# Kernel optimization log

Measured on AMD Instinct MI355X. Metric: run time of the kernel, lower is better.

## Reference

```python
import jax, jax.numpy as jnp
import numpy as np

N_MESH, N_GRID, N_EDGES, D, H = 40962, 200000, 600000, 128, 128


def layer_norm(x, g, b, eps=1e-5):
    mu = x.mean(-1, keepdims=True)
    xc = x - mu
    var = (xc * xc).mean(-1, keepdims=True)
    return xc * jax.lax.rsqrt(var + eps) * g + b


def setup_inputs() -> dict:
    key = jax.random.key(0)
    ks = jax.random.split(key, 16)
    s = 1.0 / np.sqrt(D).astype(np.float32)
    s2 = 1.0 / np.sqrt(2 * D).astype(np.float32)
    return {
        "m2g_efeat": jax.random.normal(ks[0], (N_EDGES, D), jnp.float32),
        "grid_nfeat": jax.random.normal(ks[1], (N_GRID, D), jnp.float32),
        "mesh_nfeat": jax.random.normal(ks[2], (N_MESH, D), jnp.float32),
        "src_idx": jax.random.randint(ks[3], (N_EDGES,), 0, N_MESH, jnp.int32),
        "dst_idx": jnp.sort(jax.random.randint(ks[4], (N_EDGES,), 0, N_GRID, jnp.int32)),
        # edge TMLP (first linear split across efeat/src/dst -- equals Linear on concat)
        "We": jax.random.normal(ks[5], (D, H), jnp.float32) * s,
        "Ws": jax.random.normal(ks[6], (D, H), jnp.float32) * s,
        "Wd": jax.random.normal(ks[7], (D, H), jnp.float32) * s,
        "b0": jnp.zeros((H,), jnp.float32),
        "W1e": jax.random.normal(ks[8], (H, D), jnp.float32) * s,
        "b1e": jnp.zeros((D,), jnp.float32),
        "ge": jnp.ones((D,), jnp.float32),
        "be": jnp.zeros((D,), jnp.float32),
        # node MLP: input = concat(grid_nfeat, aggregated_efeat) -> 2D
        "Wn0": jax.random.normal(ks[9], (2 * D, H), jnp.float32) * s2,
        "bn0": jnp.zeros((H,), jnp.float32),
        "Wn1": jax.random.normal(ks[10], (H, D), jnp.float32) * s,
        "bn1": jnp.zeros((D,), jnp.float32),
        "gn": jnp.ones((D,), jnp.float32),
        "bn": jnp.zeros((D,), jnp.float32),
    }


def reference(m2g_efeat, grid_nfeat, mesh_nfeat, src_idx, dst_idx,
              We, Ws, Wd, b0, W1e, b1e, ge, be,
              Wn0, bn0, Wn1, bn1, gn, bn):
    # edge TMLP: project each input tensor then gather (CUGO truncated-MLP form)
    h = jax.nn.silu(m2g_efeat @ We
                    + (mesh_nfeat @ Ws)[src_idx]
                    + (grid_nfeat @ Wd)[dst_idx]
                    + b0)                                  # [E, H]
    efeat = layer_norm(h @ W1e + b1e, ge, be)              # [E, D]
    # sum aggregation edge->node, then concat with dst node features
    agg = jax.ops.segment_sum(efeat, dst_idx, num_segments=grid_nfeat.shape[0])  # [N_grid, D]
    cat = jnp.concatenate([grid_nfeat, agg], axis=-1)      # [N_grid, 2D]
    hn = jax.nn.silu(cat @ Wn0 + bn0)                      # [N_grid, H]
    dst = layer_norm(hn @ Wn1 + bn1, gn, bn) + grid_nfeat  # residual
    return dst
```

## Files before the change

kernel.cpp:

```cpp
#include <hip/hip_runtime.h>
#include <math.h>

#define NM 40962
#define NG 200000
#define NE 600000

typedef unsigned short u16;
typedef unsigned int u32;
typedef __attribute__((ext_vector_type(8))) short short8;
typedef __attribute__((ext_vector_type(4))) float f32x4;

#define OFF_WE 0
#define OFF_WS 16384
#define OFF_WD 32768
#define OFF_W1 49152
#define OFF_W0 65536
#define OFF_WN1 98304
__device__ u16 g_wp[114688];

__device__ __forceinline__ u32 f2bf(float f) {
  u32 u = __float_as_uint(f);
  return (u + 0x7FFFu + ((u >> 16) & 1u)) >> 16;
}
__device__ __forceinline__ float bfl(u32 h) { return __uint_as_float(h << 16); }
__device__ __forceinline__ float bsel(u32 w, int hiHalf) {
  return hiHalf ? __uint_as_float(w & 0xFFFF0000u) : __uint_as_float(w << 16);
}
__device__ __forceinline__ float silu_f(float x) { return x / (1.f + __expf(-x)); }

#define MFMA16(a, b, c) __builtin_amdgcn_mfma_f32_16x16x32_bf16(a, b, c, 0, 0, 0)

__device__ __forceinline__ void pk_hl(const float* __restrict__ f, short8& hi, short8& lo) {
#pragma unroll
  for (int j = 0; j < 8; ++j) {
    u32 h = f2bf(f[j]);
    hi[j] = (short)h;
    lo[j] = (short)f2bf(f[j] - bfl(h));
  }
}

__device__ __forceinline__ void afrag_hl(const float* __restrict__ X, int row, int k0,
                                         short8& hi, short8& lo) {
  const float4* p = (const float4*)(X + (size_t)row * 128 + k0);
  float4 a = p[0], b = p[1];
  float f[8] = {a.x, a.y, a.z, a.w, b.x, b.y, b.z, b.w};
  pk_hl(f, hi, lo);
}

template <int K>
__device__ __forceinline__ short8 bfrag(const u16* __restrict__ Wp, int n, int k0) {
  return *(const short8*)(Wp + (size_t)n * K + k0);
}

__global__ void prep_kernel(const float* __restrict__ W, int off, int kbits, int total) {
  int K = 1 << kbits;
  for (int i = blockIdx.x * blockDim.x + threadIdx.x; i < total;
       i += gridDim.x * blockDim.x) {
    int n = i >> kbits, k = i & (K - 1);
    g_wp[off + i] = (u16)f2bf(W[(size_t)k * 128 + n]);
  }
}

__global__ __launch_bounds__(256) void proj_kernel(const float* __restrict__ X,
                                                   int woff, uint4* __restrict__ O,
                                                   int nrows) {
  const u16* Wp = g_wp + woff;
  const int lane = threadIdx.x & 63, wv = threadIdx.x >> 6;
  const int g = lane >> 4, c = lane & 15;
  const int nw = gridDim.x * 4;
  for (int t = blockIdx.x * 4 + wv; t * 32 < nrows; t += nw) {
    const int n0 = t * 32;
    f32x4 acc[2][8];
#pragma unroll
    for (int mt = 0; mt < 2; ++mt)
#pragma unroll
      for (int nt = 0; nt < 8; ++nt) {
        f32x4 z = {0.f, 0.f, 0.f, 0.f};
        acc[mt][nt] = z;
      }
#pragma unroll
    for (int kt = 0; kt < 4; ++kt) {
      short8 ah[2], al[2];
#pragma unroll
      for (int mt = 0; mt < 2; ++mt) {
        int row = n0 + 16 * mt + c;
        if (row >= nrows) row = nrows - 1;
        afrag_hl(X, row, 32 * kt + 8 * g, ah[mt], al[mt]);
      }
#pragma unroll
      for (int nt = 0; nt < 8; ++nt) {
        short8 b = bfrag<128>(Wp, 16 * nt + c, 32 * kt + 8 * g);
#pragma unroll
        for (int mt = 0; mt < 2; ++mt) {
          acc[mt][nt] = MFMA16(ah[mt], b, acc[mt][nt]);
          acc[mt][nt] = MFMA16(al[mt], b, acc[mt][nt]);
        }
      }
    }
#pragma unroll
    for (int mt = 0; mt < 2; ++mt)
#pragma unroll
      for (int r = 0; r < 4; ++r) {
        int row = n0 + 16 * mt + 4 * g + r;
        if (row < nrows) {
          uint4 v;
          v.x = f2bf(acc[mt][0][r]) | (f2bf(acc[mt][1][r]) << 16);
          v.y = f2bf(acc[mt][2][r]) | (f2bf(acc[mt][3][r]) << 16);
          v.z = f2bf(acc[mt][4][r]) | (f2bf(acc[mt][5][r]) << 16);
          v.w = f2bf(acc[mt][6][r]) | (f2bf(acc[mt][7][r]) << 16);
          O[(size_t)row * 16 + c] = v;
        }
      }
  }
}

__global__ __launch_bounds__(256) void edge_kernel(
    const float* __restrict__ m2g, const uint4* __restrict__ PS,
    const uint4* __restrict__ PD, const int* __restrict__ src_idx,
    const int* __restrict__ dst_idx, const float* __restrict__ b0,
    const float* __restrict__ b1e, const float* __restrict__ ge,
    const float* __restrict__ be, float* __restrict__ agg) {
  const u16* WpE = g_wp + OFF_WE;
  const u16* Wp1 = g_wp + OFF_W1;
  __shared__ __align__(16) u16 hbuf[4][2][32][128];
  const int lane = threadIdx.x & 63, wv = threadIdx.x >> 6;
  const int g = lane >> 4, c = lane & 15;
  float b0p[8], b1p[8], gep[8], bep[8];
#pragma unroll
  for (int nt = 0; nt < 8; ++nt) {
    b0p[nt] = b0[16 * nt + c];
    b1p[nt] = b1e[16 * nt + c];
    gep[nt] = ge[16 * nt + c];
    bep[nt] = be[16 * nt + c];
  }
  const int nw = gridDim.x * 4;
  for (int t = blockIdx.x * 4 + wv; t * 32 < NE; t += nw) {
    const int e0 = t * 32;
    int dd[2][4];
    uint4 ps[2][4], pd[2][4];
#pragma unroll
    for (int mt = 0; mt < 2; ++mt)
#pragma unroll
      for (int r = 0; r < 4; ++r) {
        int e = e0 + 16 * mt + 4 * g + r;
        int s = src_idx[e];
        int d = dst_idx[e];
        dd[mt][r] = d;
        ps[mt][r] = PS[(size_t)s * 16 + c];
        pd[mt][r] = PD[(size_t)d * 16 + c];
      }
    f32x4 acc[2][8];
#pragma unroll
    for (int mt = 0; mt < 2; ++mt)
#pragma unroll
      for (int nt = 0; nt < 8; ++nt) {
        f32x4 a;
#pragma unroll
        for (int r = 0; r < 4; ++r) {
          u32 pw = ((const u32*)&ps[mt][r])[nt >> 1];
          u32 qw = ((const u32*)&pd[mt][r])[nt >> 1];
          a[r] = b0p[nt] + bsel(pw, nt & 1) + bsel(qw, nt & 1);
        }
        acc[mt][nt] = a;
      }
#pragma unroll
    for (int kt = 0; kt < 4; ++kt) {
      short8 ah[2], al[2];
#pragma unroll
      for (int mt = 0; mt < 2; ++mt)
        afrag_hl(m2g, e0 + 16 * mt + c, 32 * kt + 8 * g, ah[mt], al[mt]);
#pragma unroll
      for (int nt = 0; nt < 8; ++nt) {
        short8 b = bfrag<128>(WpE, 16 * nt + c, 32 * kt + 8 * g);
#pragma unroll
        for (int mt = 0; mt < 2; ++mt) {
          acc[mt][nt] = MFMA16(ah[mt], b, acc[mt][nt]);
          acc[mt][nt] = MFMA16(al[mt], b, acc[mt][nt]);
        }
      }
    }
#pragma unroll
    for (int mt = 0; mt < 2; ++mt)
#pragma unroll
      for (int r = 0; r < 4; ++r) {
        int row = 16 * mt + 4 * g + r;
        int sw = (row & 7) << 3;
#pragma unroll
        for (int nt = 0; nt < 8; ++nt) {
          float h = silu_f(acc[mt][nt][r]);
          u32 hb = f2bf(h);
          u32 lb = f2bf(h - bfl(hb));
          int idx = (16 * nt + c) ^ sw;
          hbuf[wv][0][row][idx] = (u16)hb;
          hbuf[wv][1][row][idx] = (u16)lb;
        }
      }
    f32x4 acc2[2][8];
#pragma unroll
    for (int mt = 0; mt < 2; ++mt)
#pragma unroll
      for (int nt = 0; nt < 8; ++nt) {
        f32x4 a = {b1p[nt], b1p[nt], b1p[nt], b1p[nt]};
        acc2[mt][nt] = a;
      }
#pragma unroll
    for (int kt = 0; kt < 4; ++kt) {
      short8 ah[2], al[2];
#pragma unroll
      for (int mt = 0; mt < 2; ++mt) {
        int row = 16 * mt + c;
        int idx = (32 * kt + 8 * g) ^ ((c & 7) << 3);
        ah[mt] = *(const short8*)&hbuf[wv][0][row][idx];
        al[mt] = *(const short8*)&hbuf[wv][1][row][idx];
      }
#pragma unroll
      for (int nt = 0; nt < 8; ++nt) {
        short8 b = bfrag<128>(Wp1, 16 * nt + c, 32 * kt + 8 * g);
#pragma unroll
        for (int mt = 0; mt < 2; ++mt) {
          acc2[mt][nt] = MFMA16(ah[mt], b, acc2[mt][nt]);
          acc2[mt][nt] = MFMA16(al[mt], b, acc2[mt][nt]);
        }
      }
    }
#pragma unroll
    for (int mt = 0; mt < 2; ++mt) {
#pragma unroll
      for (int r = 0; r < 4; ++r) {
        float sm = 0.f, sq = 0.f;
#pragma unroll
        for (int nt = 0; nt < 8; ++nt) {
          float v = acc2[mt][nt][r];
          sm += v;
          sq += v * v;
        }
#pragma unroll
        for (int m = 1; m < 16; m <<= 1) {
          sm += __shfl_xor(sm, m, 64);
          sq += __shfl_xor(sq, m, 64);
        }
        float mu = sm * (1.f / 128.f);
        float var = sq * (1.f / 128.f) - mu * mu;
        float rs = rsqrtf(var + 1e-5f);
#pragma unroll
        for (int nt = 0; nt < 8; ++nt)
          acc2[mt][nt][r] = (acc2[mt][nt][r] - mu) * rs * gep[nt] + bep[nt];
      }
#pragma unroll
      for (int nt = 0; nt < 8; ++nt) {
        float a = acc2[mt][nt][0];
        int dp = dd[mt][0];
#pragma unroll
        for (int r = 1; r < 4; ++r) {
          if (dd[mt][r] == dp) {
            a += acc2[mt][nt][r];
          } else {
            atomicAdd(agg + (size_t)dp * 128 + 16 * nt + c, a);
            a = acc2[mt][nt][r];
            dp = dd[mt][r];
          }
        }
        atomicAdd(agg + (size_t)dp * 128 + 16 * nt + c, a);
      }
    }
  }
}

__global__ __launch_bounds__(256) void node_kernel(
    const float* __restrict__ gridf, const float* __restrict__ agg,
    const float* __restrict__ bn0, const float* __restrict__ bn1,
    const float* __restrict__ gn, const float* __restrict__ bnv,
    float* __restrict__ out) {
  const u16* Wp0 = g_wp + OFF_W0;
  const u16* Wp1 = g_wp + OFF_WN1;
  __shared__ __align__(16) u16 hbuf[4][32][128];
  const int lane = threadIdx.x & 63, wv = threadIdx.x >> 6;
  const int g = lane >> 4, c = lane & 15;
  float b0p[8], b1p[8], gp[8], bp[8];
#pragma unroll
  for (int nt = 0; nt < 8; ++nt) {
    b0p[nt] = bn0[16 * nt + c];
    b1p[nt] = bn1[16 * nt + c];
    gp[nt] = gn[16 * nt + c];
    bp[nt] = bnv[16 * nt + c];
  }
  const int nw = gridDim.x * 4;
  for (int t = blockIdx.x * 4 + wv; t * 32 < NG; t += nw) {
    const int n0 = t * 32;
    f32x4 acc[2][8];
#pragma unroll
    for (int mt = 0; mt < 2; ++mt)
#pragma unroll
      for (int nt = 0; nt < 8; ++nt) {
        f32x4 a = {b0p[nt], b0p[nt], b0p[nt], b0p[nt]};
        acc[mt][nt] = a;
      }
#pragma unroll
    for (int kt = 0; kt < 8; ++kt) {
      const float* src = (kt < 4) ? gridf : agg;
      int k0 = (kt & 3) * 32 + 8 * g;
      short8 ah[2], al[2];
#pragma unroll
      for (int mt = 0; mt < 2; ++mt) afrag_hl(src, n0 + 16 * mt + c, k0, ah[mt], al[mt]);
#pragma unroll
      for (int nt = 0; nt < 8; ++nt) {
        short8 b = bfrag<256>(Wp0, 16 * nt + c, 32 * kt + 8 * g);
#pragma unroll
        for (int mt = 0; mt < 2; ++mt) {
          acc[mt][nt] = MFMA16(ah[mt], b, acc[mt][nt]);
          acc[mt][nt] = MFMA16(al[mt], b, acc[mt][nt]);
        }
      }
    }
#pragma unroll
    for (int mt = 0; mt < 2; ++mt)
#pragma unroll
      for (int r = 0; r < 4; ++r) {
        int row = 16 * mt + 4 * g + r;
        int sw = (row & 7) << 3;
#pragma unroll
        for (int nt = 0; nt < 8; ++nt)
          hbuf[wv][row][(16 * nt + c) ^ sw] = (u16)f2bf(silu_f(acc[mt][nt][r]));
      }
    f32x4 acc2[2][8];
#pragma unroll
    for (int mt = 0; mt < 2; ++mt)
#pragma unroll
      for (int nt = 0; nt < 8; ++nt) {
        f32x4 a = {b1p[nt], b1p[nt], b1p[nt], b1p[nt]};
        acc2[mt][nt] = a;
      }
#pragma unroll
    for (int kt = 0; kt < 4; ++kt) {
      short8 ah[2];
#pragma unroll
      for (int mt = 0; mt < 2; ++mt) {
        int row = 16 * mt + c;
        ah[mt] = *(const short8*)&hbuf[wv][row][(32 * kt + 8 * g) ^ ((c & 7) << 3)];
      }
#pragma unroll
      for (int nt = 0; nt < 8; ++nt) {
        short8 b = bfrag<128>(Wp1, 16 * nt + c, 32 * kt + 8 * g);
#pragma unroll
        for (int mt = 0; mt < 2; ++mt) acc2[mt][nt] = MFMA16(ah[mt], b, acc2[mt][nt]);
      }
    }
#pragma unroll
    for (int mt = 0; mt < 2; ++mt)
#pragma unroll
      for (int r = 0; r < 4; ++r) {
        float sm = 0.f, sq = 0.f;
#pragma unroll
        for (int nt = 0; nt < 8; ++nt) {
          float v = acc2[mt][nt][r];
          sm += v;
          sq += v * v;
        }
#pragma unroll
        for (int m = 1; m < 16; m <<= 1) {
          sm += __shfl_xor(sm, m, 64);
          sq += __shfl_xor(sq, m, 64);
        }
        float mu = sm * (1.f / 128.f);
        float var = sq * (1.f / 128.f) - mu * mu;
        float rs = rsqrtf(var + 1e-5f);
        int row = n0 + 16 * mt + 4 * g + r;
#pragma unroll
        for (int nt = 0; nt < 8; ++nt) {
          size_t o = (size_t)row * 128 + 16 * nt + c;
          out[o] = (acc2[mt][nt][r] - mu) * rs * gp[nt] + bp[nt] + gridf[o];
        }
      }
  }
}

extern "C" void kernel_launch(void* const* d_in, const int* in_sizes, int n_in,
                              void* d_out, int out_size, void* d_ws, size_t ws_size,
                              hipStream_t stream) {
  const float* m2g = (const float*)d_in[0];
  const float* grid = (const float*)d_in[1];
  const float* mesh = (const float*)d_in[2];
  const int* src = (const int*)d_in[3];
  const int* dst = (const int*)d_in[4];
  const float* We = (const float*)d_in[5];
  const float* Ws = (const float*)d_in[6];
  const float* Wd = (const float*)d_in[7];
  const float* b0 = (const float*)d_in[8];
  const float* W1e = (const float*)d_in[9];
  const float* b1e = (const float*)d_in[10];
  const float* ge = (const float*)d_in[11];
  const float* be = (const float*)d_in[12];
  const float* Wn0 = (const float*)d_in[13];
  const float* bn0 = (const float*)d_in[14];
  const float* Wn1 = (const float*)d_in[15];
  const float* bn1 = (const float*)d_in[16];
  const float* gn = (const float*)d_in[17];
  const float* bnv = (const float*)d_in[18];
  (void)in_sizes; (void)n_in; (void)out_size; (void)ws_size;

  char* ws = (char*)d_ws;
  float* agg = (float*)ws;
  size_t aggB = (size_t)NG * 128 * 4;
  size_t psB = (size_t)NM * 256;
  uint4* PS = (uint4*)(ws + aggB);
  uint4* PD = (uint4*)(ws + aggB + psB);

  prep_kernel<<<64, 256, 0, stream>>>(We, OFF_WE, 7, 16384);
  prep_kernel<<<64, 256, 0, stream>>>(Ws, OFF_WS, 7, 16384);
  prep_kernel<<<64, 256, 0, stream>>>(Wd, OFF_WD, 7, 16384);
  prep_kernel<<<64, 256, 0, stream>>>(W1e, OFF_W1, 7, 16384);
  prep_kernel<<<128, 256, 0, stream>>>(Wn0, OFF_W0, 8, 32768);
  prep_kernel<<<64, 256, 0, stream>>>(Wn1, OFF_WN1, 7, 16384);
  hipMemsetAsync(agg, 0, aggB, stream);
  proj_kernel<<<512, 256, 0, stream>>>(mesh, OFF_WS, PS, NM);
  proj_kernel<<<512, 256, 0, stream>>>(grid, OFF_WD, PD, NG);
  edge_kernel<<<512, 256, 0, stream>>>(m2g, PS, PD, src, dst, b0, b1e, ge, be, agg);
  node_kernel<<<512, 256, 0, stream>>>(grid, agg, bn0, bn1, gn, bnv, (float*)d_out);
}
```

Measured before the change: 1.230 ms.

## Merge prep/proj launches, halve LDS staging and raise occupancy in edge/node kernels

Folds the six weight-prep launches into one kernel and the two projection launches into one combined-range kernel, cutting launch overhead. The edge and node kernels now run the second GEMM and layernorm one 16-row half at a time. This halves the shared-memory staging buffer (hi/lo bf16 packed into one u32) and the live accumulator registers, and LN gamma/beta loads move inside the loop. Launch bounds of 3 blocks/SM and larger grids aim for more waves in flight to hide gather and atomic latency. The risk is register spills or extra scalar loads from forcing the occupancy target.

```diff
diff --git a/kernel.cpp b/kernel.cpp
--- a/kernel.cpp
+++ b/kernel.cpp
@@ -52,24 +52,40 @@
   return *(const short8*)(Wp + (size_t)n * K + k0);
 }
 
-__global__ void prep_kernel(const float* __restrict__ W, int off, int kbits, int total) {
-  int K = 1 << kbits;
-  for (int i = blockIdx.x * blockDim.x + threadIdx.x; i < total;
+__global__ void prep_all(const float* __restrict__ We, const float* __restrict__ Ws,
+                         const float* __restrict__ Wd, const float* __restrict__ W1e,
+                         const float* __restrict__ Wn0, const float* __restrict__ Wn1) {
+  for (int i = blockIdx.x * blockDim.x + threadIdx.x; i < 114688;
        i += gridDim.x * blockDim.x) {
-    int n = i >> kbits, k = i & (K - 1);
-    g_wp[off + i] = (u16)f2bf(W[(size_t)k * 128 + n]);
-  }
-}
-
-__global__ __launch_bounds__(256) void proj_kernel(const float* __restrict__ X,
-                                                   int woff, uint4* __restrict__ O,
-                                                   int nrows) {
-  const u16* Wp = g_wp + woff;
+    const float* W;
+    int loc, kb;
+    if (i < 16384)       { W = We;  loc = i;         kb = 7; }
+    else if (i < 32768)  { W = Ws;  loc = i - 16384; kb = 7; }
+    else if (i < 49152)  { W = Wd;  loc = i - 32768; kb = 7; }
+    else if (i < 65536)  { W = W1e; loc = i - 49152; kb = 7; }
+    else if (i < 98304)  { W = Wn0; loc = i - 65536; kb = 8; }
+    else                 { W = Wn1; loc = i - 98304; kb = 7; }
+    int n = loc >> kb, k = loc & ((1 << kb) - 1);
+    g_wp[i] = (u16)f2bf(W[(size_t)k * 128 + n]);
+  }
+}
+
+__global__ __launch_bounds__(256, 3) void proj_kernel(const float* __restrict__ mesh,
+                                                      const float* __restrict__ gridf,
+                                                      uint4* __restrict__ PS,
+                                                      uint4* __restrict__ PD) {
+  const int TM = (NM + 31) / 32;
+  const int TG = NG / 32;
   const int lane = threadIdx.x & 63, wv = threadIdx.x >> 6;
   const int g = lane >> 4, c = lane & 15;
   const int nw = gridDim.x * 4;
-  for (int t = blockIdx.x * 4 + wv; t * 32 < nrows; t += nw) {
-    const int n0 = t * 32;
+  for (int t = blockIdx.x * 4 + wv; t < TM + TG; t += nw) {
+    const float* X;
+    const u16* Wp;
+    uint4* O;
+    int n0, nrows;
+    if (t < TM) { X = mesh;  Wp = g_wp + OFF_WS; O = PS; n0 = t * 32;        nrows = NM; }
+    else        { X = gridf; Wp = g_wp + OFF_WD; O = PD; n0 = (t - TM) * 32; nrows = NG; }
     f32x4 acc[2][8];
 #pragma unroll
     for (int mt = 0; mt < 2; ++mt)
@@ -114,7 +130,7 @@
   }
 }
 
-__global__ __launch_bounds__(256) void edge_kernel(
+__global__ __launch_bounds__(256, 3) void edge_kernel(
     const float* __restrict__ m2g, const uint4* __restrict__ PS,
     const uint4* __restrict__ PD, const int* __restrict__ src_idx,
     const int* __restrict__ dst_idx, const float* __restrict__ b0,
@@ -122,47 +138,47 @@
     const float* __restrict__ be, float* __restrict__ agg) {
   const u16* WpE = g_wp + OFF_WE;
   const u16* Wp1 = g_wp + OFF_W1;
-  __shared__ __align__(16) u16 hbuf[4][2][32][128];
+  __shared__ __align__(16) u32 hbuf[4][16][128];
   const int lane = threadIdx.x & 63, wv = threadIdx.x >> 6;
   const int g = lane >> 4, c = lane & 15;
-  float b0p[8], b1p[8], gep[8], bep[8];
+  float b0p[8], b1p[8];
 #pragma unroll
   for (int nt = 0; nt < 8; ++nt) {
     b0p[nt] = b0[16 * nt + c];
     b1p[nt] = b1e[16 * nt + c];
-    gep[nt] = ge[16 * nt + c];
-    bep[nt] = be[16 * nt + c];
   }
   const int nw = gridDim.x * 4;
   for (int t = blockIdx.x * 4 + wv; t * 32 < NE; t += nw) {
     const int e0 = t * 32;
     int dd[2][4];
-    uint4 ps[2][4], pd[2][4];
-#pragma unroll
-    for (int mt = 0; mt < 2; ++mt)
-#pragma unroll
-      for (int r = 0; r < 4; ++r) {
-        int e = e0 + 16 * mt + 4 * g + r;
-        int s = src_idx[e];
-        int d = dst_idx[e];
-        dd[mt][r] = d;
-        ps[mt][r] = PS[(size_t)s * 16 + c];
-        pd[mt][r] = PD[(size_t)d * 16 + c];
-      }
     f32x4 acc[2][8];
-#pragma unroll
-    for (int mt = 0; mt < 2; ++mt)
-#pragma unroll
-      for (int nt = 0; nt < 8; ++nt) {
-        f32x4 a;
+    {
+      uint4 ps[2][4], pd[2][4];
+#pragma unroll
+      for (int mt = 0; mt < 2; ++mt)
 #pragma unroll
         for (int r = 0; r < 4; ++r) {
-          u32 pw = ((const u32*)&ps[mt][r])[nt >> 1];
-          u32 qw = ((const u32*)&pd[mt][r])[nt >> 1];
-          a[r] = b0p[nt] + bsel(pw, nt & 1) + bsel(qw, nt & 1);
-        }
-        acc[mt][nt] = a;
-      }
+          int e = e0 + 16 * mt + 4 * g + r;
+          int s = src_idx[e];
+          int d = dst_idx[e];
+          dd[mt][r] = d;
+          ps[mt][r] = PS[(size_t)s * 16 + c];
+          pd[mt][r] = PD[(size_t)d * 16 + c];
+        }
+#pragma unroll
+      for (int mt = 0; mt < 2; ++mt)
+#pragma unroll
+        for (int nt = 0; nt < 8; ++nt) {
+          f32x4 a;
+#pragma unroll
+          for (int r = 0; r < 4; ++r) {
+            u32 pw = ((const u32*)&ps[mt][r])[nt >> 1];
+            u32 qw = ((const u32*)&pd[mt][r])[nt >> 1];
+            a[r] = b0p[nt] + bsel(pw, nt & 1) + bsel(qw, nt & 1);
+          }
+          acc[mt][nt] = a;
+        }
+    }
 #pragma unroll
     for (int kt = 0; kt < 4; ++kt) {
       short8 ah[2], al[2];
@@ -180,57 +196,56 @@
       }
     }
 #pragma unroll
-    for (int mt = 0; mt < 2; ++mt)
+    for (int mt = 0; mt < 2; ++mt) {
 #pragma unroll
       for (int r = 0; r < 4; ++r) {
-        int row = 16 * mt + 4 * g + r;
+        int row = 4 * g + r;
         int sw = (row & 7) << 3;
 #pragma unroll
         for (int nt = 0; nt < 8; ++nt) {
           float h = silu_f(acc[mt][nt][r]);
           u32 hb = f2bf(h);
           u32 lb = f2bf(h - bfl(hb));
-          int idx = (16 * nt + c) ^ sw;
-          hbuf[wv][0][row][idx] = (u16)hb;
-          hbuf[wv][1][row][idx] = (u16)lb;
-        }
-      }
-    f32x4 acc2[2][8];
-#pragma unroll
-    for (int mt = 0; mt < 2; ++mt)
+          hbuf[wv][row][(16 * nt + c) ^ sw] = hb | (lb << 16);
+        }
+      }
+      f32x4 acc2[8];
 #pragma unroll
       for (int nt = 0; nt < 8; ++nt) {
         f32x4 a = {b1p[nt], b1p[nt], b1p[nt], b1p[nt]};
-        acc2[mt][nt] = a;
-      }
-#pragma unroll
-    for (int kt = 0; kt < 4; ++kt) {
-      short8 ah[2], al[2];
-#pragma unroll
-      for (int mt = 0; mt < 2; ++mt) {
-        int row = 16 * mt + c;
-        int idx = (32 * kt + 8 * g) ^ ((c & 7) << 3);
-        ah[mt] = *(const short8*)&hbuf[wv][0][row][idx];
-        al[mt] = *(const short8*)&hbuf[wv][1][row][idx];
-      }
-#pragma unroll
-      for (int nt = 0; nt < 8; ++nt) {
-        short8 b = bfrag<128>(Wp1, 16 * nt + c, 32 * kt + 8 * g);
-#pragma unroll
-        for (int mt = 0; mt < 2; ++mt) {
-          acc2[mt][nt] = MFMA16(ah[mt], b, acc2[mt][nt]);
-          acc2[mt][nt] = MFMA16(al[mt], b, acc2[mt][nt]);
-        }
-      }
-    }
-#pragma unroll
-    for (int mt = 0; mt < 2; ++mt) {
+        acc2[nt] = a;
+      }
+#pragma unroll
+      for (int kt = 0; kt < 4; ++kt) {
+        const u32* hp = &hbuf[wv][c][(32 * kt + 8 * g) ^ ((c & 7) << 3)];
+        uint4 w0 = *(const uint4*)hp;
+        uint4 w1 = *(const uint4*)(hp + 4);
+        u32 wsv[8] = {w0.x, w0.y, w0.z, w0.w, w1.x, w1.y, w1.z, w1.w};
+        short8 ah, al;
+#pragma unroll
+        for (int j = 0; j < 8; ++j) {
+          ah[j] = (short)(wsv[j] & 0xFFFFu);
+          al[j] = (short)(wsv[j] >> 16);
+        }
+#pragma unroll
+        for (int nt = 0; nt < 8; ++nt) {
+          short8 b = bfrag<128>(Wp1, 16 * nt + c, 32 * kt + 8 * g);
+          acc2[nt] = MFMA16(ah, b, acc2[nt]);
+          acc2[nt] = MFMA16(al, b, acc2[nt]);
+        }
+      }
+      float gep[8], bep[8];
+#pragma unroll
+      for (int nt = 0; nt < 8; ++nt) {
+        gep[nt] = ge[16 * nt + c];
+        bep[nt] = be[16 * nt + c];
+      }
 #pragma unroll
       for (int r = 0; r < 4; ++r) {
         float sm = 0.f, sq = 0.f;
 #pragma unroll
         for (int nt = 0; nt < 8; ++nt) {
-          float v = acc2[mt][nt][r];
+          float v = acc2[nt][r];
           sm += v;
           sq += v * v;
         }
@@ -244,19 +259,19 @@
         float rs = rsqrtf(var + 1e-5f);
 #pragma unroll
         for (int nt = 0; nt < 8; ++nt)
-          acc2[mt][nt][r] = (acc2[mt][nt][r] - mu) * rs * gep[nt] + bep[nt];
-      }
-#pragma unroll
-      for (int nt = 0; nt < 8; ++nt) {
-        float a = acc2[mt][nt][0];
+          acc2[nt][r] = (acc2[nt][r] - mu) * rs * gep[nt] + bep[nt];
+      }
+#pragma unroll
+      for (int nt = 0; nt < 8; ++nt) {
+        float a = acc2[nt][0];
         int dp = dd[mt][0];
 #pragma unroll
         for (int r = 1; r < 4; ++r) {
           if (dd[mt][r] == dp) {
-            a += acc2[mt][nt][r];
+            a += acc2[nt][r];
           } else {
             atomicAdd(agg + (size_t)dp * 128 + 16 * nt + c, a);
-            a = acc2[mt][nt][r];
+            a = acc2[nt][r];
             dp = dd[mt][r];
           }
         }
@@ -266,23 +281,21 @@
   }
 }
 
-__global__ __launch_bounds__(256) void node_kernel(
+__global__ __launch_bounds__(256, 3) void node_kernel(
     const float* __restrict__ gridf, const float* __restrict__ agg,
     const float* __restrict__ bn0, const float* __restrict__ bn1,
     const float* __restrict__ gn, const float* __restrict__ bnv,
     float* __restrict__ out) {
   const u16* Wp0 = g_wp + OFF_W0;
   const u16* Wp1 = g_wp + OFF_WN1;
-  __shared__ __align__(16) u16 hbuf[4][32][128];
+  __shared__ __align__(16) u16 nbuf[4][16][128];
   const int lane = threadIdx.x & 63, wv = threadIdx.x >> 6;
   const int g = lane >> 4, c = lane & 15;
-  float b0p[8], b1p[8], gp[8], bp[8];
+  float b0p[8], b1p[8];
 #pragma unroll
   for (int nt = 0; nt < 8; ++nt) {
     b0p[nt] = bn0[16 * nt + c];
     b1p[nt] = bn1[16 * nt + c];
-    gp[nt] = gn[16 * nt + c];
-    bp[nt] = bnv[16 * nt + c];
   }
   const int nw = gridDim.x * 4;
   for (int t = blockIdx.x * 4 + wv; t * 32 < NG; t += nw) {
@@ -313,46 +326,42 @@
       }
     }
 #pragma unroll
-    for (int mt = 0; mt < 2; ++mt)
+    for (int mt = 0; mt < 2; ++mt) {
 #pragma unroll
       for (int r = 0; r < 4; ++r) {
-        int row = 16 * mt + 4 * g + r;
+        int row = 4 * g + r;
         int sw = (row & 7) << 3;
 #pragma unroll
         for (int nt = 0; nt < 8; ++nt)
-          hbuf[wv][row][(16 * nt + c) ^ sw] = (u16)f2bf(silu_f(acc[mt][nt][r]));
-      }
-    f32x4 acc2[2][8];
-#pragma unroll
-    for (int mt = 0; mt < 2; ++mt)
+          nbuf[wv][row][(16 * nt + c) ^ sw] = (u16)f2bf(silu_f(acc[mt][nt][r]));
+      }
+      f32x4 acc2[8];
 #pragma unroll
       for (int nt = 0; nt < 8; ++nt) {
         f32x4 a = {b1p[nt], b1p[nt], b1p[nt], b1p[nt]};
-        acc2[mt][nt] = a;
-      }
-#pragma unroll
-    for (int kt = 0; kt < 4; ++kt) {
-      short8 ah[2];
-#pragma unroll
-      for (int mt = 0; mt < 2; ++mt) {
-        int row = 16 * mt + c;
-        ah[mt] = *(const short8*)&hbuf[wv][row][(32 * kt + 8 * g) ^ ((c & 7) << 3)];
-      }
-#pragma unroll
-      for (int nt = 0; nt < 8; ++nt) {
-        short8 b = bfrag<128>(Wp1, 16 * nt + c, 32 * kt + 8 * g);
-#pragma unroll
-        for (int mt = 0; mt < 2; ++mt) acc2[mt][nt] = MFMA16(ah[mt], b, acc2[mt][nt]);
-      }
-    }
-#pragma unroll
-    for (int mt = 0; mt < 2; ++mt)
+        acc2[nt] = a;
+      }
+#pragma unroll
+      for (int kt = 0; kt < 4; ++kt) {
+        short8 ah = *(const short8*)&nbuf[wv][c][(32 * kt + 8 * g) ^ ((c & 7) << 3)];
+#pragma unroll
+        for (int nt = 0; nt < 8; ++nt) {
+          short8 b = bfrag<128>(Wp1, 16 * nt + c, 32 * kt + 8 * g);
+          acc2[nt] = MFMA16(ah, b, acc2[nt]);
+        }
+      }
+      float gp[8], bp[8];
+#pragma unroll
+      for (int nt = 0; nt < 8; ++nt) {
+        gp[nt] = gn[16 * nt + c];
+        bp[nt] = bnv[16 * nt + c];
+      }
 #pragma unroll
       for (int r = 0; r < 4; ++r) {
         float sm = 0.f, sq = 0.f;
 #pragma unroll
         for (int nt = 0; nt < 8; ++nt) {
-          float v = acc2[mt][nt][r];
+          float v = acc2[nt][r];
           sm += v;
           sq += v * v;
         }
@@ -368,9 +377,10 @@
 #pragma unroll
         for (int nt = 0; nt < 8; ++nt) {
           size_t o = (size_t)row * 128 + 16 * nt + c;
-          out[o] = (acc2[mt][nt][r] - mu) * rs * gp[nt] + bp[nt] + gridf[o];
-        }
-      }
+          out[o] = (acc2[nt][r] - mu) * rs * gp[nt] + bp[nt] + gridf[o];
+        }
+      }
+    }
   }
 }
 
@@ -405,15 +415,9 @@
   uint4* PS = (uint4*)(ws + aggB);
   uint4* PD = (uint4*)(ws + aggB + psB);
 
-  prep_kernel<<<64, 256, 0, stream>>>(We, OFF_WE, 7, 16384);
-  prep_kernel<<<64, 256, 0, stream>>>(Ws, OFF_WS, 7, 16384);
-  prep_kernel<<<64, 256, 0, stream>>>(Wd, OFF_WD, 7, 16384);
-  prep_kernel<<<64, 256, 0, stream>>>(W1e, OFF_W1, 7, 16384);
-  prep_kernel<<<128, 256, 0, stream>>>(Wn0, OFF_W0, 8, 32768);
-  prep_kernel<<<64, 256, 0, stream>>>(Wn1, OFF_WN1, 7, 16384);
+  prep_all<<<224, 256, 0, stream>>>(We, Ws, Wd, W1e, Wn0, Wn1);
   hipMemsetAsync(agg, 0, aggB, stream);
-  proj_kernel<<<512, 256, 0, stream>>>(mesh, OFF_WS, PS, NM);
-  proj_kernel<<<512, 256, 0, stream>>>(grid, OFF_WD, PD, NG);
-  edge_kernel<<<512, 256, 0, stream>>>(m2g, PS, PD, src, dst, b0, b1e, ge, be, agg);
-  node_kernel<<<512, 256, 0, stream>>>(grid, agg, bn0, bn1, gn, bnv, (float*)d_out);
-}
+  proj_kernel<<<1024, 256, 0, stream>>>(mesh, grid, PS, PD);
+  edge_kernel<<<1536, 256, 0, stream>>>(m2g, PS, PD, src, dst, b0, b1e, ge, be, agg);
+  node_kernel<<<1536, 256, 0, stream>>>(grid, agg, bn0, bn1, gn, bnv, (float*)d_out);
+}
```

After: 1.711 ms. +39.1%, slower.
